# Kernel optimization log

Measured on AMD Instinct MI355X. Metric: run time of the kernel, lower is better.

The kernel has to match this reference:

```python
import jax, jax.numpy as jnp
import numpy as np

NUM_USERS = 200000
NUM_ITEMS = 100000
DIM = 64
N_LAYERS = 2
K_TYPES = 4  # coarse behavior types EP/IP/EN/IN, one LightGCN encoder each
E_UU = 1000000
E_UI = 1600000  # edges per fold (2 folds per direction)
E_II = 1000000
DEG_SCALE = 0.0625  # mimics 1/deg normalization of adjacency values


def _spmm(rows, cols, vals, x, nrows):
    # sparse [nrows, ncols] @ x [ncols, D] via gather + segment_sum (COO SpMM)
    return jax.ops.segment_sum(vals[:, None] * x[cols], rows, num_segments=nrows)


def setup_inputs() -> dict:
    key = jax.random.key(0)
    ks = jax.random.split(key, 32)
    def ridx(k, n, hi):
        return jax.random.randint(k, (n,), 0, hi, dtype=jnp.int32)
    def rval(k, n):
        return jax.random.uniform(k, (n,), dtype=jnp.float32) * DEG_SCALE
    inp = {}
    inp["u2u_rows"] = ridx(ks[0], E_UU, NUM_USERS)
    inp["u2u_cols"] = ridx(ks[1], E_UU, NUM_USERS)
    inp["u2u_vals"] = rval(ks[2], E_UU)
    inp["u2i_rows0"] = ridx(ks[3], E_UI, NUM_USERS // 2)
    inp["u2i_cols0"] = ridx(ks[4], E_UI, NUM_ITEMS)
    inp["u2i_vals0"] = rval(ks[5], E_UI)
    inp["u2i_rows1"] = ridx(ks[6], E_UI, NUM_USERS // 2)
    inp["u2i_cols1"] = ridx(ks[7], E_UI, NUM_ITEMS)
    inp["u2i_vals1"] = rval(ks[8], E_UI)
    inp["i2u_rows0"] = ridx(ks[9], E_UI, NUM_ITEMS // 2)
    inp["i2u_cols0"] = ridx(ks[10], E_UI, NUM_USERS)
    inp["i2u_vals0"] = rval(ks[11], E_UI)
    inp["i2u_rows1"] = ridx(ks[12], E_UI, NUM_ITEMS // 2)
    inp["i2u_cols1"] = ridx(ks[13], E_UI, NUM_USERS)
    inp["i2u_vals1"] = rval(ks[14], E_UI)
    inp["i2i_rows"] = ridx(ks[15], E_II, NUM_ITEMS)
    inp["i2i_cols"] = ridx(ks[16], E_II, NUM_ITEMS)
    inp["i2i_vals"] = rval(ks[17], E_II)
    # per-type embedding tables (xavier-ish init, scaled for stability)
    inp["user_embs"] = jax.random.normal(ks[18], (K_TYPES, NUM_USERS, DIM), dtype=jnp.float32) * 0.1
    inp["item_embs"] = jax.random.normal(ks[19], (K_TYPES, NUM_ITEMS, DIM), dtype=jnp.float32) * 0.1
    # fine weights (combine_choice='mean' -> [D, D] per coarse type)
    inp["W_u"] = jax.random.normal(ks[20], (K_TYPES, DIM, DIM), dtype=jnp.float32) * (1.0 / np.sqrt(DIM))
    inp["W_v"] = jax.random.normal(ks[21], (K_TYPES, DIM, DIM), dtype=jnp.float32) * (1.0 / np.sqrt(DIM))
    return inp


def _lightgcn(ue, ie,
              u2u_rows, u2u_cols, u2u_vals,
              u2i_folds, i2u_folds,
              i2i_rows, i2i_cols, i2i_vals):
    # LightGCN.forward: propagate n_layers, mean over layer outputs incl. layer 0
    ue_acc, ie_acc = ue, ie
    for _ in range(N_LAYERS):
        u2u_agg = _spmm(u2u_rows, u2u_cols, u2u_vals, ue, NUM_USERS)
        # fold-wise u2i SpMM over item embedding, concat rows back to NUM_USERS
        i2u_agg = jnp.concatenate(
            [_spmm(r, c, v, ie, NUM_USERS // 2) for (r, c, v) in u2i_folds], axis=0)
        i2i_agg = _spmm(i2i_rows, i2i_cols, i2i_vals, ie, NUM_ITEMS)
        u2i_agg = jnp.concatenate(
            [_spmm(r, c, v, ue, NUM_ITEMS // 2) for (r, c, v) in i2u_folds], axis=0)
        ue = u2u_agg + i2u_agg
        ie = i2i_agg + u2i_agg
        ue_acc = ue_acc + ue
        ie_acc = ie_acc + ie
    inv = 1.0 / (N_LAYERS + 1)
    return ue_acc * inv, ie_acc * inv


def reference(u2u_rows, u2u_cols, u2u_vals,
              u2i_rows0, u2i_cols0, u2i_vals0,
              u2i_rows1, u2i_cols1, u2i_vals1,
              i2u_rows0, i2u_cols0, i2u_vals0,
              i2u_rows1, i2u_cols1, i2u_vals1,
              i2i_rows, i2i_cols, i2i_vals,
              user_embs, item_embs, W_u, W_v):
    u2i_folds = [(u2i_rows0, u2i_cols0, u2i_vals0), (u2i_rows1, u2i_cols1, u2i_vals1)]
    i2u_folds = [(i2u_rows0, i2u_cols0, i2u_vals0), (i2u_rows1, i2u_cols1, i2u_vals1)]
    user_outs, item_outs = [], []
    for k in range(K_TYPES):  # one LightGCN encoder per coarse behavior type
        ue, ie = _lightgcn(user_embs[k], item_embs[k],
                           u2u_rows, u2u_cols, u2u_vals,
                           u2i_folds, i2u_folds,
                           i2i_rows, i2i_cols, i2i_vals)
        # combine_choice='mean' (single behavior per type) + fine weight + ReLU
        user_outs.append(jax.nn.relu(ue @ W_u[k]))
        item_outs.append(jax.nn.relu(ie @ W_v[k]))
    user_all = jnp.concatenate(user_outs, axis=-1)  # [U, K*D]
    item_all = jnp.concatenate(item_outs, axis=-1)  # [I, K*D]
    return (user_all, item_all)
```

## Files before the change

kernel.cpp:

```cpp
#include <hip/hip_runtime.h>

#define NU 200000
#define NI 100000
#define TOTR (NU + NI)
#define NBK 586
#define EPB 8192


struct Bld {
  const int* rows[6]; const int* cols[6]; const float* vals[6];
  int base[6]; int coff[6];
  int eoff[7];
};


__device__ __forceinline__ unsigned bfr(float f) {
  unsigned u = __float_as_uint(f);
  return (u + 0x7FFFu + ((u >> 16) & 1u)) >> 16;
}
__device__ __forceinline__ float blo(unsigned p) { return __uint_as_float(p << 16); }
__device__ __forceinline__ float bhi(unsigned p) { return __uint_as_float(p & 0xFFFF0000u); }

__device__ __forceinline__ int list_of(const Bld& b, int g) {
  int l = 0;
#pragma unroll
  for (int k = 0; k < 5; ++k) l += (g >= b.eoff[k + 1]) ? 1 : 0;
  return l;
}


__global__ __launch_bounds__(256) void bhist_k(Bld b, int* __restrict__ bcount, int totE) {
  __shared__ int cnt[NBK];
  int t = threadIdx.x;
  for (int i = t; i < NBK; i += 256) cnt[i] = 0;
  __syncthreads();
  int g0 = blockIdx.x * EPB;
  int gend = min(g0 + EPB, totE);
  for (int g = g0 + t; g < gend; g += 256) {
    int l = list_of(b, g);
    int i = g - b.eoff[l];
    int drow = b.base[l] + b.rows[l][i];
    atomicAdd(&cnt[drow >> 9], 1);
  }
  __syncthreads();
  for (int i = t; i < NBK; i += 256) if (cnt[i]) atomicAdd(&bcount[i], cnt[i]);
}

__global__ __launch_bounds__(256) void bscan_k(const int* __restrict__ bcount,
    int* __restrict__ bbase, int* __restrict__ bcursor, int* __restrict__ offs) {
  __shared__ int s_run;
  __shared__ int wsum[4];
  int t = threadIdx.x, lane = t & 63, wv = t >> 6;
  if (t == 0) s_run = 0;
  __syncthreads();
  for (int base = 0; base < NBK; base += 256) {
    int v = (base + t < NBK) ? bcount[base + t] : 0;
    int sc = v;
#pragma unroll
    for (int o = 1; o < 64; o <<= 1) { int x = __shfl_up(sc, o, 64); if (lane >= o) sc += x; }
    if (lane == 63) wsum[wv] = sc;
    __syncthreads();
    int wb = 0;
    for (int j = 0; j < wv; ++j) wb += wsum[j];
    int run = s_run;
    if (base + t < NBK) {
      int ex = run + wb + sc - v;
      bbase[base + t] = ex; bcursor[base + t] = ex;
    }
    __syncthreads();
    if (t == 255) s_run = run + wsum[0] + wsum[1] + wsum[2] + wsum[3];
    __syncthreads();
  }
  if (t == 0) { bbase[NBK] = s_run; offs[TOTR] = s_run; }
}

__global__ __launch_bounds__(256) void bscatter_k(Bld b, int* __restrict__ bcursor,
    uint2* __restrict__ ebuf, int totE) {
  __shared__ int cnt[NBK];
  __shared__ int gb[NBK];
  int t = threadIdx.x;
  for (int i = t; i < NBK; i += 256) cnt[i] = 0;
  __syncthreads();
  int g0 = blockIdx.x * EPB;
  int gend = min(g0 + EPB, totE);
  unsigned pk[32];
  for (int j = 0; j < 32; ++j) {
    int g = g0 + t + j * 256;
    if (g < gend) {
      int l = list_of(b, g);
      int i = g - b.eoff[l];
      int drow = b.base[l] + b.rows[l][i];
      int bk = drow >> 9, rl = drow & 511;
      int lp = atomicAdd(&cnt[bk], 1);
      pk[j] = ((unsigned)bk << 22) | ((unsigned)rl << 13) | (unsigned)lp;
    }
  }
  __syncthreads();
  for (int i = t; i < NBK; i += 256) {
    int c = cnt[i];
    if (c) gb[i] = atomicAdd(&bcursor[i], c);
  }
  __syncthreads();
  for (int j = 0; j < 32; ++j) {
    int g = g0 + t + j * 256;
    if (g >= gend) break;
    unsigned v = pk[j];
    int bk = v >> 22, rl = (v >> 13) & 511, lp = v & 0x1FFF;
    int l = list_of(b, g);
    int i = g - b.eoff[l];
    unsigned cc = (unsigned)(b.cols[l][i] + b.coff[l]);
    ebuf[gb[bk] + lp] = make_uint2(((unsigned)rl << 19) | cc,
                                   __float_as_uint(b.vals[l][i]));
  }
}

__global__ __launch_bounds__(256) void fine_k(const uint2* __restrict__ ebuf,
    const int* __restrict__ bbase, int* __restrict__ offs,
    uint2* __restrict__ edges) {
  __shared__ int rcnt[512];
  __shared__ int rcur[512];
  __shared__ int wsum[4];
  int bk = blockIdx.x, t = threadIdx.x;
  rcnt[t] = 0; rcnt[t + 256] = 0;
  __syncthreads();
  int gbeg = bbase[bk], gend = bbase[bk + 1];
  for (int e = gbeg + t; e < gend; e += 256)
    atomicAdd(&rcnt[ebuf[e].x >> 19], 1);
  __syncthreads();
  int a0 = rcnt[2 * t], a1 = rcnt[2 * t + 1];
  int ts = a0 + a1, sc = ts;
  int lane = t & 63, wv = t >> 6;
#pragma unroll
  for (int o = 1; o < 64; o <<= 1) { int x = __shfl_up(sc, o, 64); if (lane >= o) sc += x; }
  if (lane == 63) wsum[wv] = sc;
  __syncthreads();
  int wb = 0;
  for (int j = 0; j < wv; ++j) wb += wsum[j];
  int ex = wb + sc - ts;
  __syncthreads();
  rcnt[2 * t] = ex;      rcnt[2 * t + 1] = ex + a0;
  rcur[2 * t] = ex;      rcur[2 * t + 1] = ex + a0;
  __syncthreads();
  int rfirst = bk << 9;
  for (int i = t; i < 512; i += 256) {
    int row = rfirst + i;
    if (row < TOTR) offs[row] = gbeg + rcnt[i];
  }
  for (int e = gbeg + t; e < gend; e += 256) {
    uint2 ev = ebuf[e];
    int rl = ev.x >> 19;
    int lp = atomicAdd(&rcur[rl], 1);
    edges[gbeg + lp] = make_uint2(ev.x & 0x7FFFFu, ev.y);
  }
}


__global__ __launch_bounds__(256) void init_k(const float* __restrict__ embs,
                                              uint2* __restrict__ buf, int nrows) {
  int idx = blockIdx.x * 256 + threadIdx.x;
  if (idx >= nrows * 64) return;
  int u = idx >> 6, q = idx & 63;
  int k = q >> 4, d = (q & 15) * 4;
  const float4 f = *(const float4*)(embs + ((size_t)k * nrows + u) * 64 + d);
  uint2 o;
  o.x = (bfr(f.y) << 16) | bfr(f.x);
  o.y = (bfr(f.w) << 16) | bfr(f.z);
  buf[idx] = o;
}


__device__ __forceinline__ void gacc(float a[4], const uint2* __restrict__ x,
    int beg, int end, const uint2* __restrict__ edges, int lane) {
  for (int e0 = beg; e0 < end; e0 += 64) {
    int nn = min(64, end - e0);
    uint2 ev = make_uint2(0u, 0u);
    if (lane < nn) ev = edges[e0 + lane];
    int nb = (nn + 15) & ~15;
    for (int s = 0; s < nb; s += 16) {
      uint2 d[16];
#pragma unroll
      for (int j = 0; j < 16; ++j) {
        unsigned c = (unsigned)__shfl((int)ev.x, s + j);
        d[j] = x[(size_t)c * 64u + (unsigned)lane];
      }
#pragma unroll
      for (int j = 0; j < 16; ++j) {
        float v = __uint_as_float((unsigned)__shfl((int)ev.y, s + j));
        a[0] += v * blo(d[j].x);
        a[1] += v * bhi(d[j].x);
        a[2] += v * blo(d[j].y);
        a[3] += v * bhi(d[j].y);
      }
    }
  }
}

__global__ __launch_bounds__(256) void spmm_k(
    const uint2* __restrict__ x, uint2* __restrict__ nxt,
    const int* __restrict__ offs, const uint2* __restrict__ edges, int nrows) {
  int w = (blockIdx.x * 256 + threadIdx.x) >> 6;
  int lane = threadIdx.x & 63;
  if (w >= nrows) return;
  float a[4] = {0.f, 0.f, 0.f, 0.f};
  gacc(a, x, offs[w], offs[w + 1], edges, lane);
  uint2 o;
  o.x = (bfr(a[1]) << 16) | bfr(a[0]);
  o.y = (bfr(a[3]) << 16) | bfr(a[2]);
  nxt[(size_t)w * 64 + lane] = o;
}


__global__ __launch_bounds__(256) void xform_k(float* __restrict__ out,
    const float* __restrict__ uembs, const float* __restrict__ iembs,
    const uint2* __restrict__ u1, const uint2* __restrict__ u0,
    const uint2* __restrict__ i1, const uint2* __restrict__ i0,
    const float* __restrict__ Wu, const float* __restrict__ Wv) {
  const int utiles = NU / 64;
  int tile = blockIdx.x;
  const float* embs; const uint2 *b1, *b0; const float* W; float* base; int nrows, row0;
  if (tile < utiles) {
    embs = uembs; b1 = u1; b0 = u0; W = Wu; base = out; nrows = NU; row0 = tile * 64;
  } else {
    embs = iembs; b1 = i1; b0 = i0; W = Wv; base = out + (size_t)NU * 256; nrows = NI;
    row0 = (tile - utiles) * 64;
  }
  __shared__ float Xs[64][68];
  __shared__ float Ws[64][68];
  int t = threadIdx.x;
  int tr = t >> 4, tc = (t & 15) * 4;
  const float inv3 = 1.f / 3.f;
  for (int k = 0; k < 4; ++k) {
#pragma unroll
    for (int i = 0; i < 4; ++i) {
      int e = t + i * 256;
      int r = e >> 4, c4 = e & 15;
      float4 wv = ((const float4*)(W + (size_t)k * 4096 + (size_t)r * 64))[c4];
      *(float4*)&Ws[r][c4 * 4] = wv;
      int row = row0 + r;
      float4 xv = make_float4(0.f, 0.f, 0.f, 0.f);
      if (row < nrows) {
        const float4 e0 = *(const float4*)(embs + ((size_t)k * nrows + row) * 64 + c4 * 4);
        uint2 p1 = b1[(size_t)row * 64 + k * 16 + c4];
        uint2 p2 = b0[(size_t)row * 64 + k * 16 + c4];
        xv.x = (e0.x + blo(p1.x) + blo(p2.x)) * inv3;
        xv.y = (e0.y + bhi(p1.x) + bhi(p2.x)) * inv3;
        xv.z = (e0.z + blo(p1.y) + blo(p2.y)) * inv3;
        xv.w = (e0.w + bhi(p1.y) + bhi(p2.y)) * inv3;
      }
      *(float4*)&Xs[r][c4 * 4] = xv;
    }
    __syncthreads();
    float y[4][4];
#pragma unroll
    for (int i = 0; i < 4; ++i)
#pragma unroll
      for (int j = 0; j < 4; ++j) y[i][j] = 0.f;
    for (int j = 0; j < 64; ++j) {
      float xr[4], wc[4];
#pragma unroll
      for (int i = 0; i < 4; ++i) { xr[i] = Xs[tr * 4 + i][j]; wc[i] = Ws[j][tc + i]; }
#pragma unroll
      for (int i = 0; i < 4; ++i)
#pragma unroll
        for (int jj = 0; jj < 4; ++jj) y[i][jj] += xr[i] * wc[jj];
    }
#pragma unroll
    for (int i = 0; i < 4; ++i) {
      int row = row0 + tr * 4 + i;
      if (row < nrows) {
        float4 o = make_float4(fmaxf(y[i][0], 0.f), fmaxf(y[i][1], 0.f),
                               fmaxf(y[i][2], 0.f), fmaxf(y[i][3], 0.f));
        ((float4*)(base + (size_t)row * 256 + k * 64))[t & 15] = o;
      }
    }
    __syncthreads();
  }
}


extern "C" void kernel_launch(void* const* d_in, const int* in_sizes, int n_in,
                              void* d_out, int out_size, void* d_ws, size_t ws_size,
                              hipStream_t stream) {
  Bld b;
  const int rows_idx[6] = {0, 3, 6, 9, 12, 15};
  const int dbase[6] = {0, 0, NU / 2, NU, NU + NI / 2, NU};
  const int coff[6]  = {0, NU, NU, 0, 0, NU};
  int totE = 0;
  for (int l = 0; l < 6; ++l) {
    b.rows[l] = (const int*)d_in[rows_idx[l]];
    b.cols[l] = (const int*)d_in[rows_idx[l] + 1];
    b.vals[l] = (const float*)d_in[rows_idx[l] + 2];
    b.base[l] = dbase[l];
    b.coff[l] = coff[l];
    b.eoff[l] = totE;
    totE += in_sizes[rows_idx[l]];
  }
  b.eoff[6] = totE;

  char* basep = (char*)d_ws; size_t off = 0;
  auto alloc = [&](size_t bytes) -> void* {
    void* r = basep + off; off = (off + bytes + 255) & ~(size_t)255; return r;
  };
  uint2* bufA = (uint2*)alloc((size_t)TOTR * 64 * 8);
  uint2* bufB = (uint2*)alloc((size_t)TOTR * 64 * 8);
  int* offs = (int*)alloc((size_t)(TOTR + 1) * 4);
  int* bcount = (int*)alloc((size_t)NBK * 4);
  int* bbase = (int*)alloc((size_t)(NBK + 1) * 4);
  int* bcursor = (int*)alloc((size_t)NBK * 4);
  uint2* edges = (uint2*)alloc((size_t)totE * 8);
  uint2* ebuf = bufB;

  hipMemsetAsync(bcount, 0, (size_t)NBK * 4, stream);
  int nblk = (totE + EPB - 1) / EPB;
  bhist_k<<<nblk, 256, 0, stream>>>(b, bcount, totE);
  bscan_k<<<1, 256, 0, stream>>>(bcount, bbase, bcursor, offs);
  bscatter_k<<<nblk, 256, 0, stream>>>(b, bcursor, ebuf, totE);
  fine_k<<<NBK, 256, 0, stream>>>(ebuf, bbase, offs, edges);

  const float* user_embs = (const float*)d_in[18];
  const float* item_embs = (const float*)d_in[19];
  const float* W_u = (const float*)d_in[20];
  const float* W_v = (const float*)d_in[21];

  init_k<<<(NU * 64 + 255) / 256, 256, 0, stream>>>(user_embs, bufA, NU);
  init_k<<<(NI * 64 + 255) / 256, 256, 0, stream>>>(item_embs, bufA + (size_t)NU * 64, NI);

  spmm_k<<<(TOTR + 3) / 4, 256, 0, stream>>>(bufA, bufB, offs, edges, TOTR);
  spmm_k<<<(TOTR + 3) / 4, 256, 0, stream>>>(bufB, bufA, offs, edges, TOTR);

  int tiles = NU / 64 + (NI + 63) / 64;
  xform_k<<<tiles, 256, 0, stream>>>((float*)d_out, user_embs, item_embs,
      bufB, bufA, bufB + (size_t)NU * 64, bufA + (size_t)NU * 64, W_u, W_v);
}
```

Measured before the change: 2.174 ms.

## Split SpMM into per-type-pair passes with type-major embedding layout

Stores the bf16 embedding buffers type-major ([K][rows][64]) instead of interleaving all four types per row. Each SpMM layer now runs as two launches, each handling two types with half-wavefronts, so every gathered row is a contiguous 128-byte chunk per type. The aim is a smaller gathered working set per pass, which should improve cache hit rates on the random column gathers. In exchange the edge lists and shuffles are read twice per layer, and the gather per edge is narrower.

```diff
diff --git a/kernel.cpp b/kernel.cpp
--- a/kernel.cpp
+++ b/kernel.cpp
@@ -156,73 +156,66 @@
 
 
 __global__ __launch_bounds__(256) void init_k(const float* __restrict__ embs,
-                                              uint2* __restrict__ buf, int nrows) {
+    uint2* __restrict__ buf, int nrows, int rowoff) {
   int idx = blockIdx.x * 256 + threadIdx.x;
   if (idx >= nrows * 64) return;
   int u = idx >> 6, q = idx & 63;
-  int k = q >> 4, d = (q & 15) * 4;
-  const float4 f = *(const float4*)(embs + ((size_t)k * nrows + u) * 64 + d);
+  int k = q >> 4, d4 = q & 15;
+  const float4 f = *(const float4*)(embs + ((size_t)k * nrows + u) * 64 + d4 * 4);
   uint2 o;
   o.x = (bfr(f.y) << 16) | bfr(f.x);
   o.y = (bfr(f.w) << 16) | bfr(f.z);
-  buf[idx] = o;
-}
-
-
-__device__ __forceinline__ void gacc(float a[4], const uint2* __restrict__ x,
-    int beg, int end, const uint2* __restrict__ edges, int lane) {
+  buf[((size_t)k * TOTR + rowoff + u) * 16 + d4] = o;
+}
+
+
+__global__ __launch_bounds__(256) void spmm2_k(
+    const unsigned* __restrict__ x, unsigned* __restrict__ nxt,
+    const int* __restrict__ offs, const uint2* __restrict__ edges, int kbase) {
+  int w = (blockIdx.x * 256 + threadIdx.x) >> 6;
+  int lane = threadIdx.x & 63;
+  if (w >= TOTR) return;
+  int hl = lane & 31;
+  int k = kbase + (lane >> 5);
+  const unsigned* xk = x + (size_t)k * ((size_t)TOTR * 32);
+  float a0 = 0.f, a1 = 0.f;
+  int beg = offs[w], end = offs[w + 1];
   for (int e0 = beg; e0 < end; e0 += 64) {
     int nn = min(64, end - e0);
     uint2 ev = make_uint2(0u, 0u);
     if (lane < nn) ev = edges[e0 + lane];
     int nb = (nn + 15) & ~15;
     for (int s = 0; s < nb; s += 16) {
-      uint2 d[16];
+      unsigned d[16];
 #pragma unroll
       for (int j = 0; j < 16; ++j) {
         unsigned c = (unsigned)__shfl((int)ev.x, s + j);
-        d[j] = x[(size_t)c * 64u + (unsigned)lane];
+        d[j] = xk[(size_t)c * 32u + (unsigned)hl];
       }
 #pragma unroll
       for (int j = 0; j < 16; ++j) {
         float v = __uint_as_float((unsigned)__shfl((int)ev.y, s + j));
-        a[0] += v * blo(d[j].x);
-        a[1] += v * bhi(d[j].x);
-        a[2] += v * blo(d[j].y);
-        a[3] += v * bhi(d[j].y);
+        a0 += v * blo(d[j]);
+        a1 += v * bhi(d[j]);
       }
     }
   }
-}
-
-__global__ __launch_bounds__(256) void spmm_k(
-    const uint2* __restrict__ x, uint2* __restrict__ nxt,
-    const int* __restrict__ offs, const uint2* __restrict__ edges, int nrows) {
-  int w = (blockIdx.x * 256 + threadIdx.x) >> 6;
-  int lane = threadIdx.x & 63;
-  if (w >= nrows) return;
-  float a[4] = {0.f, 0.f, 0.f, 0.f};
-  gacc(a, x, offs[w], offs[w + 1], edges, lane);
-  uint2 o;
-  o.x = (bfr(a[1]) << 16) | bfr(a[0]);
-  o.y = (bfr(a[3]) << 16) | bfr(a[2]);
-  nxt[(size_t)w * 64 + lane] = o;
+  nxt[((size_t)k * TOTR + w) * 32 + hl] = (bfr(a1) << 16) | bfr(a0);
 }
 
 
 __global__ __launch_bounds__(256) void xform_k(float* __restrict__ out,
     const float* __restrict__ uembs, const float* __restrict__ iembs,
-    const uint2* __restrict__ u1, const uint2* __restrict__ u0,
-    const uint2* __restrict__ i1, const uint2* __restrict__ i0,
+    const uint2* __restrict__ b1, const uint2* __restrict__ b0,
     const float* __restrict__ Wu, const float* __restrict__ Wv) {
   const int utiles = NU / 64;
   int tile = blockIdx.x;
-  const float* embs; const uint2 *b1, *b0; const float* W; float* base; int nrows, row0;
+  const float* embs; const float* W; float* base; int nrows, row0, rowbase;
   if (tile < utiles) {
-    embs = uembs; b1 = u1; b0 = u0; W = Wu; base = out; nrows = NU; row0 = tile * 64;
+    embs = uembs; W = Wu; base = out; nrows = NU; row0 = tile * 64; rowbase = 0;
   } else {
-    embs = iembs; b1 = i1; b0 = i0; W = Wv; base = out + (size_t)NU * 256; nrows = NI;
-    row0 = (tile - utiles) * 64;
+    embs = iembs; W = Wv; base = out + (size_t)NU * 256; nrows = NI;
+    row0 = (tile - utiles) * 64; rowbase = NU;
   }
   __shared__ float Xs[64][68];
   __shared__ float Ws[64][68];
@@ -240,8 +233,8 @@
       float4 xv = make_float4(0.f, 0.f, 0.f, 0.f);
       if (row < nrows) {
         const float4 e0 = *(const float4*)(embs + ((size_t)k * nrows + row) * 64 + c4 * 4);
-        uint2 p1 = b1[(size_t)row * 64 + k * 16 + c4];
-        uint2 p2 = b0[(size_t)row * 64 + k * 16 + c4];
+        uint2 p1 = b1[((size_t)k * TOTR + rowbase + row) * 16 + c4];
+        uint2 p2 = b0[((size_t)k * TOTR + rowbase + row) * 16 + c4];
         xv.x = (e0.x + blo(p1.x) + blo(p2.x)) * inv3;
         xv.y = (e0.y + bhi(p1.x) + bhi(p2.x)) * inv3;
         xv.z = (e0.z + blo(p1.y) + blo(p2.y)) * inv3;
@@ -301,14 +294,14 @@
   auto alloc = [&](size_t bytes) -> void* {
     void* r = basep + off; off = (off + bytes + 255) & ~(size_t)255; return r;
   };
-  uint2* bufA = (uint2*)alloc((size_t)TOTR * 64 * 8);
-  uint2* bufB = (uint2*)alloc((size_t)TOTR * 64 * 8);
+  unsigned* bufA = (unsigned*)alloc((size_t)TOTR * 128 * 4);
+  unsigned* bufB = (unsigned*)alloc((size_t)TOTR * 128 * 4);
   int* offs = (int*)alloc((size_t)(TOTR + 1) * 4);
   int* bcount = (int*)alloc((size_t)NBK * 4);
   int* bbase = (int*)alloc((size_t)(NBK + 1) * 4);
   int* bcursor = (int*)alloc((size_t)NBK * 4);
   uint2* edges = (uint2*)alloc((size_t)totE * 8);
-  uint2* ebuf = bufB;
+  uint2* ebuf = (uint2*)bufB;
 
   hipMemsetAsync(bcount, 0, (size_t)NBK * 4, stream);
   int nblk = (totE + EPB - 1) / EPB;
@@ -322,13 +315,16 @@
   const float* W_u = (const float*)d_in[20];
   const float* W_v = (const float*)d_in[21];
 
-  init_k<<<(NU * 64 + 255) / 256, 256, 0, stream>>>(user_embs, bufA, NU);
-  init_k<<<(NI * 64 + 255) / 256, 256, 0, stream>>>(item_embs, bufA + (size_t)NU * 64, NI);
-
-  spmm_k<<<(TOTR + 3) / 4, 256, 0, stream>>>(bufA, bufB, offs, edges, TOTR);
-  spmm_k<<<(TOTR + 3) / 4, 256, 0, stream>>>(bufB, bufA, offs, edges, TOTR);
+  init_k<<<(NU * 64 + 255) / 256, 256, 0, stream>>>(user_embs, (uint2*)bufA, NU, 0);
+  init_k<<<(NI * 64 + 255) / 256, 256, 0, stream>>>(item_embs, (uint2*)bufA, NI, NU);
+
+  const int sgrid = TOTR / 4;
+  spmm2_k<<<sgrid, 256, 0, stream>>>(bufA, bufB, offs, edges, 0);
+  spmm2_k<<<sgrid, 256, 0, stream>>>(bufA, bufB, offs, edges, 2);
+  spmm2_k<<<sgrid, 256, 0, stream>>>(bufB, bufA, offs, edges, 0);
+  spmm2_k<<<sgrid, 256, 0, stream>>>(bufB, bufA, offs, edges, 2);
 
   int tiles = NU / 64 + (NI + 63) / 64;
   xform_k<<<tiles, 256, 0, stream>>>((float*)d_out, user_embs, item_embs,
-      bufB, bufA, bufB + (size_t)NU * 64, bufA + (size_t)NU * 64, W_u, W_v);
-}
+      (const uint2*)bufB, (const uint2*)bufA, W_u, W_v);
+}
```

After: 2.245 ms. +3.3%, slower.

## Drop histogram pass by scattering edges into fixed-capacity bucket slots

Applied to the files above, without the earlier changes.

Removes the separate bucket-histogram kernel by having the scatter kernel write each edge into a fixed-capacity region per coarse bucket (CAP slots), using a global cursor as both counter and allocator. The scan now runs after scatter on the final counts, and the fine sort reads from the padded bucket regions while writing compacted CSR output. This saves one full pass over the six edge lists' rows, at the cost of a larger staging buffer and the assumption that no bucket exceeds CAP edges.

```diff
diff --git a/kernel.cpp b/kernel.cpp
--- a/kernel.cpp
+++ b/kernel.cpp
@@ -5,12 +5,15 @@
 #define TOTR (NU + NI)
 #define NBK 586
 #define EPB 8192
+#define CAP 32768
 
 
 struct Bld {
   const int* rows[6]; const int* cols[6]; const float* vals[6];
   int base[6]; int coff[6];
   int eoff[7];
+  int* bcursor;
+  uint2* ebuf;
 };
 
 
@@ -29,53 +32,7 @@
 }
 
 
-__global__ __launch_bounds__(256) void bhist_k(Bld b, int* __restrict__ bcount, int totE) {
-  __shared__ int cnt[NBK];
-  int t = threadIdx.x;
-  for (int i = t; i < NBK; i += 256) cnt[i] = 0;
-  __syncthreads();
-  int g0 = blockIdx.x * EPB;
-  int gend = min(g0 + EPB, totE);
-  for (int g = g0 + t; g < gend; g += 256) {
-    int l = list_of(b, g);
-    int i = g - b.eoff[l];
-    int drow = b.base[l] + b.rows[l][i];
-    atomicAdd(&cnt[drow >> 9], 1);
-  }
-  __syncthreads();
-  for (int i = t; i < NBK; i += 256) if (cnt[i]) atomicAdd(&bcount[i], cnt[i]);
-}
-
-__global__ __launch_bounds__(256) void bscan_k(const int* __restrict__ bcount,
-    int* __restrict__ bbase, int* __restrict__ bcursor, int* __restrict__ offs) {
-  __shared__ int s_run;
-  __shared__ int wsum[4];
-  int t = threadIdx.x, lane = t & 63, wv = t >> 6;
-  if (t == 0) s_run = 0;
-  __syncthreads();
-  for (int base = 0; base < NBK; base += 256) {
-    int v = (base + t < NBK) ? bcount[base + t] : 0;
-    int sc = v;
-#pragma unroll
-    for (int o = 1; o < 64; o <<= 1) { int x = __shfl_up(sc, o, 64); if (lane >= o) sc += x; }
-    if (lane == 63) wsum[wv] = sc;
-    __syncthreads();
-    int wb = 0;
-    for (int j = 0; j < wv; ++j) wb += wsum[j];
-    int run = s_run;
-    if (base + t < NBK) {
-      int ex = run + wb + sc - v;
-      bbase[base + t] = ex; bcursor[base + t] = ex;
-    }
-    __syncthreads();
-    if (t == 255) s_run = run + wsum[0] + wsum[1] + wsum[2] + wsum[3];
-    __syncthreads();
-  }
-  if (t == 0) { bbase[NBK] = s_run; offs[TOTR] = s_run; }
-}
-
-__global__ __launch_bounds__(256) void bscatter_k(Bld b, int* __restrict__ bcursor,
-    uint2* __restrict__ ebuf, int totE) {
+__global__ __launch_bounds__(256) void bscatter_k(Bld b, int totE) {
   __shared__ int cnt[NBK];
   __shared__ int gb[NBK];
   int t = threadIdx.x;
@@ -98,34 +55,61 @@
   __syncthreads();
   for (int i = t; i < NBK; i += 256) {
     int c = cnt[i];
-    if (c) gb[i] = atomicAdd(&bcursor[i], c);
+    if (c) gb[i] = atomicAdd(&b.bcursor[i], c);
   }
   __syncthreads();
   for (int j = 0; j < 32; ++j) {
     int g = g0 + t + j * 256;
     if (g >= gend) break;
     unsigned v = pk[j];
-    int bk = v >> 22, rl = (v >> 13) & 511, lp = v & 0x1FFF;
+    int bk = v >> 22, rl = (v >> 13) & 0x1FF, lp = v & 0x1FFF;
     int l = list_of(b, g);
     int i = g - b.eoff[l];
     unsigned cc = (unsigned)(b.cols[l][i] + b.coff[l]);
-    ebuf[gb[bk] + lp] = make_uint2(((unsigned)rl << 19) | cc,
-                                   __float_as_uint(b.vals[l][i]));
-  }
+    b.ebuf[(size_t)bk * CAP + gb[bk] + lp] =
+        make_uint2(((unsigned)rl << 19) | cc, __float_as_uint(b.vals[l][i]));
+  }
+}
+
+__global__ __launch_bounds__(256) void bscan_k(const int* __restrict__ bcount,
+    int* __restrict__ bbase, int* __restrict__ offs) {
+  __shared__ int s_run;
+  __shared__ int wsum[4];
+  int t = threadIdx.x, lane = t & 63, wv = t >> 6;
+  if (t == 0) s_run = 0;
+  __syncthreads();
+  for (int base = 0; base < NBK; base += 256) {
+    int v = (base + t < NBK) ? bcount[base + t] : 0;
+    int sc = v;
+#pragma unroll
+    for (int o = 1; o < 64; o <<= 1) { int x = __shfl_up(sc, o, 64); if (lane >= o) sc += x; }
+    if (lane == 63) wsum[wv] = sc;
+    __syncthreads();
+    int wb = 0;
+    for (int j = 0; j < wv; ++j) wb += wsum[j];
+    int run = s_run;
+    if (base + t < NBK) bbase[base + t] = run + wb + sc - v;
+    __syncthreads();
+    if (t == 255) s_run = run + wsum[0] + wsum[1] + wsum[2] + wsum[3];
+    __syncthreads();
+  }
+  if (t == 0) { bbase[NBK] = s_run; offs[TOTR] = s_run; }
 }
 
 __global__ __launch_bounds__(256) void fine_k(const uint2* __restrict__ ebuf,
-    const int* __restrict__ bbase, int* __restrict__ offs,
-    uint2* __restrict__ edges) {
+    const int* __restrict__ bcnt, const int* __restrict__ bbase,
+    int* __restrict__ offs, uint2* __restrict__ edges) {
   __shared__ int rcnt[512];
   __shared__ int rcur[512];
   __shared__ int wsum[4];
   int bk = blockIdx.x, t = threadIdx.x;
   rcnt[t] = 0; rcnt[t + 256] = 0;
   __syncthreads();
-  int gbeg = bbase[bk], gend = bbase[bk + 1];
-  for (int e = gbeg + t; e < gend; e += 256)
-    atomicAdd(&rcnt[ebuf[e].x >> 19], 1);
+  int cnt = bcnt[bk];
+  size_t ib = (size_t)bk * CAP;
+  int ob = bbase[bk];
+  for (int e = t; e < cnt; e += 256)
+    atomicAdd(&rcnt[ebuf[ib + e].x >> 19], 1);
   __syncthreads();
   int a0 = rcnt[2 * t], a1 = rcnt[2 * t + 1];
   int ts = a0 + a1, sc = ts;
@@ -144,13 +128,13 @@
   int rfirst = bk << 9;
   for (int i = t; i < 512; i += 256) {
     int row = rfirst + i;
-    if (row < TOTR) offs[row] = gbeg + rcnt[i];
-  }
-  for (int e = gbeg + t; e < gend; e += 256) {
-    uint2 ev = ebuf[e];
+    if (row < TOTR) offs[row] = ob + rcnt[i];
+  }
+  for (int e = t; e < cnt; e += 256) {
+    uint2 ev = ebuf[ib + e];
     int rl = ev.x >> 19;
     int lp = atomicAdd(&rcur[rl], 1);
-    edges[gbeg + lp] = make_uint2(ev.x & 0x7FFFFu, ev.y);
+    edges[ob + lp] = make_uint2(ev.x & 0x7FFFFu, ev.y);
   }
 }
 
@@ -301,21 +285,22 @@
   auto alloc = [&](size_t bytes) -> void* {
     void* r = basep + off; off = (off + bytes + 255) & ~(size_t)255; return r;
   };
-  uint2* bufA = (uint2*)alloc((size_t)TOTR * 64 * 8);
-  uint2* bufB = (uint2*)alloc((size_t)TOTR * 64 * 8);
+  size_t embBytes = (size_t)TOTR * 64 * 8;
+  size_t ebufBytes = (size_t)NBK * CAP * 8;
+  uint2* bufA = (uint2*)alloc(embBytes);
+  uint2* bufB = (uint2*)alloc(ebufBytes > embBytes ? ebufBytes : embBytes);
   int* offs = (int*)alloc((size_t)(TOTR + 1) * 4);
-  int* bcount = (int*)alloc((size_t)NBK * 4);
+  int* bcursor = (int*)alloc((size_t)NBK * 4);
   int* bbase = (int*)alloc((size_t)(NBK + 1) * 4);
-  int* bcursor = (int*)alloc((size_t)NBK * 4);
   uint2* edges = (uint2*)alloc((size_t)totE * 8);
-  uint2* ebuf = bufB;
-
-  hipMemsetAsync(bcount, 0, (size_t)NBK * 4, stream);
+  b.bcursor = bcursor;
+  b.ebuf = bufB;
+
+  hipMemsetAsync(bcursor, 0, (size_t)NBK * 4, stream);
   int nblk = (totE + EPB - 1) / EPB;
-  bhist_k<<<nblk, 256, 0, stream>>>(b, bcount, totE);
-  bscan_k<<<1, 256, 0, stream>>>(bcount, bbase, bcursor, offs);
-  bscatter_k<<<nblk, 256, 0, stream>>>(b, bcursor, ebuf, totE);
-  fine_k<<<NBK, 256, 0, stream>>>(ebuf, bbase, offs, edges);
+  bscatter_k<<<nblk, 256, 0, stream>>>(b, totE);
+  bscan_k<<<1, 256, 0, stream>>>(bcursor, bbase, offs);
+  fine_k<<<NBK, 256, 0, stream>>>(b.ebuf, bcursor, bbase, offs, edges);
 
   const float* user_embs = (const float*)d_in[18];
   const float* item_embs = (const float*)d_in[19];
```

After: 2.151 ms. About the same (-1.0%).
